# Optimization experiments

Hardware: AMD Instinct MI355X
Metric: run time of the kernel (lower is better)

Reference implementation:

```python
import jax, jax.numpy as jnp
import numpy as np

M = 2048      # mention groups (spans with antecedents)
K_MAX = 128   # max antecedents per mention
N = 4096      # candidate span pool
G = 1000      # span representation dim
D = 20        # distance/genre/speaker embed dim
H = 150       # Score MLP hidden
GIJ = 3 * G + 3 * D  # 3060


def setup_inputs() -> dict:
    key = jax.random.key(0)
    ks = jax.random.split(key, 12)
    # ragged group lengths (deterministic): cycle 1..K_MAX, sum = P = 132096
    lengths = np.tile(np.arange(1, K_MAX + 1), M // K_MAX).astype(np.int32)
    P = int(lengths.sum())
    seg_ids = np.repeat(np.arange(M), lengths).astype(np.int32)
    starts = np.cumsum(lengths) - lengths
    offsets = (np.arange(P) - starts[seg_ids]).astype(np.int32)

    genre_emb = jax.random.normal(ks[3], (8, D), jnp.float32) * 0.02
    genre_emb = genre_emb.at[0].set(0.0)   # padding_idx=0
    speaker_emb = jax.random.normal(ks[4], (3, D), jnp.float32) * 0.02
    speaker_emb = speaker_emb.at[0].set(0.0)  # padding_idx=0

    return {
        "g_i": jax.random.normal(ks[0], (N, G), jnp.float32),
        "mention_scores": jax.random.normal(ks[1], (N, 1), jnp.float32),
        "dist_emb": jax.random.normal(ks[2], (9, D), jnp.float32) * 0.02,
        "genre_emb": genre_emb,
        "speaker_emb": speaker_emb,
        "W1": jax.random.normal(ks[5], (GIJ, H), jnp.float32) / np.sqrt(GIJ),
        "b1": jnp.zeros((H,), jnp.float32),
        "W2": jax.random.normal(ks[6], (H, H), jnp.float32) / np.sqrt(H),
        "b2": jnp.zeros((H,), jnp.float32),
        "W3": jax.random.normal(ks[7], (H, 1), jnp.float32) / np.sqrt(H),
        "b3": jnp.zeros((1,), jnp.float32),
        "mention_ids": jax.random.randint(ks[8], (P,), 0, N, jnp.int32),
        "antecedent_ids": jax.random.randint(ks[9], (P,), 0, N, jnp.int32),
        "dist_ids": jax.random.randint(ks[10], (P,), 0, 9, jnp.int32),
        "genre_ids": jax.random.randint(ks[11], (P,), 0, 8, jnp.int32),
        "speaker_ids": jax.random.randint(jax.random.fold_in(key, 99), (P,), 0, 3, jnp.int32),
        "lengths": jnp.asarray(lengths),
        "seg_ids": jnp.asarray(seg_ids),
        "offsets": jnp.asarray(offsets),
    }


def reference(g_i, mention_scores, dist_emb, genre_emb, speaker_emb,
              W1, b1, W2, b2, W3, b3,
              mention_ids, antecedent_ids, dist_ids, genre_ids, speaker_ids,
              lengths, seg_ids, offsets):
    # feature gathers: phi = [distance, genre, speaker] embeddings, (P, 3D)
    phi = jnp.concatenate(
        [dist_emb[dist_ids], genre_emb[genre_ids], speaker_emb[speaker_ids]], axis=1)
    i_g = g_i[mention_ids]      # (P, G)
    j_g = g_i[antecedent_ids]   # (P, G)
    pairs = jnp.concatenate([i_g, j_g, i_g * j_g, phi], axis=1)  # (P, GIJ)

    # 3-layer scoring MLP (dropout inactive at eval)
    h = jax.nn.relu(pairs @ W1 + b1)
    h = jax.nn.relu(h @ W2 + b2)
    s_ij = (h @ W3 + b3)[:, 0]  # (P,)

    scores = mention_scores[mention_ids, 0] + mention_scores[antecedent_ids, 0] + s_ij

    # per-group softmax over [group scores, epsilon=0] via segment ops
    seg_max = jax.ops.segment_max(scores, seg_ids, num_segments=M)
    m = jnp.maximum(seg_max, 0.0)                      # include epsilon 0
    e = jnp.exp(scores - m[seg_ids])                   # (P,)
    eps_e = jnp.exp(-m)                                # (M,)
    denom = jax.ops.segment_sum(e, seg_ids, num_segments=M) + eps_e
    pair_probs = e / denom[seg_ids]                    # (P,)
    eps_probs = eps_e / denom                          # (M,)

    # pad_and_stack(value=1000): row 0 is the empty leading group -> [1, 1000...]
    grid = jnp.full((M + 1, K_MAX + 1), 1000.0, dtype=scores.dtype)
    grid = grid.at[seg_ids + 1, offsets].set(pair_probs)
    grid = grid.at[jnp.arange(M) + 1, lengths].set(eps_probs)
    grid = grid.at[0, 0].set(1.0)
    return grid
```

## Files before the change

### kernel.cpp

```cpp
#include <hip/hip_runtime.h>

#define P_TOTAL 132096
#define NPOOL   4096
#define GDIM    1000
#define HDIM    150
#define MGRP    2048
#define KMAX    128

typedef __attribute__((ext_vector_type(4))) float f32x4;
typedef __attribute__((ext_vector_type(2))) float f32x2;
typedef __attribute__((ext_vector_type(4))) unsigned int u32x4;

#define OFF_W1C8   0
#define OFF_W1AB8  163840
#define OFF_W2F8   491520
#define OFF_ABPRE  517120
#define OFF_TABS2  3138560
#define OFF_SGRID  3276800
#define OFF_GF8    4325376
#define OFF_ITAB   8519680

__device__ __forceinline__ short f2bf(float f) {
  union { float f; unsigned u; } v; v.f = f;
  unsigned r = v.u + 0x7FFFu + ((v.u >> 16) & 1u);
  return (short)(r >> 16);
}
__device__ __forceinline__ float bf2f(unsigned short s) {
  return __builtin_bit_cast(float, ((unsigned)s) << 16);
}
__device__ __forceinline__ unsigned char f2fp8(float f) {
  int d = __builtin_amdgcn_cvt_pk_fp8_f32(f, 0.f, 0, false);
  return (unsigned char)(d & 0xFF);
}
__device__ __forceinline__ long mk64(unsigned lo, unsigned hi) {
  return (long)(((unsigned long long)hi << 32) | lo);
}

__device__ __forceinline__ u32x4 fp8prod16(u32x4 m, u32x4 a) {
  u32x4 r;
  #pragma unroll
  for (int d = 0; d < 4; ++d) {
    f32x2 ml = __builtin_amdgcn_cvt_pk_f32_fp8(m[d], false);
    f32x2 mh = __builtin_amdgcn_cvt_pk_f32_fp8(m[d], true);
    f32x2 al = __builtin_amdgcn_cvt_pk_f32_fp8(a[d], false);
    f32x2 ah = __builtin_amdgcn_cvt_pk_f32_fp8(a[d], true);
    f32x2 pl = ml * al, ph = mh * ah;
    int o = __builtin_amdgcn_cvt_pk_fp8_f32(pl[0], pl[1], 0, false);
    o = __builtin_amdgcn_cvt_pk_fp8_f32(ph[0], ph[1], o, true);
    r[d] = (unsigned)o;
  }
  return r;
}

#define S1 5120
#define S2 10240
#define S3 800
#define S4 (NPOOL*256)
#define S5 (216*160)
#define S6 P_TOTAL
__global__ __launch_bounds__(256) void prep_kernel(
    const float* __restrict__ W1, const float* __restrict__ W2,
    const float* __restrict__ g_i,
    const float* __restrict__ dist_emb, const float* __restrict__ genre_emb,
    const float* __restrict__ spk_emb, const float* __restrict__ b1,
    const int* __restrict__ did, const int* __restrict__ gid,
    const int* __restrict__ sid,
    unsigned char* __restrict__ w1c8, unsigned char* __restrict__ w1ab8,
    unsigned char* __restrict__ w2f8, unsigned* __restrict__ gf8,
    float* __restrict__ tabs2, unsigned char* __restrict__ itab8) {
  int idx = blockIdx.x * 256 + threadIdx.x;
  if (idx < S1) {
    int c = idx / 160, n = idx % 160;
    int s = c >> 1, j = c & 1;
    unsigned dw[8];
    #pragma unroll
    for (int d = 0; d < 8; ++d) {
      unsigned acc = 0;
      #pragma unroll
      for (int b = 0; b < 4; ++b) {
        int kk = d*4 + b;
        int g = kk >> 3, i = kk & 7;
        int q = g ^ ((n >> 2) & 3);
        int k = s*64 + q*16 + j*8 + i;
        float v = (k < GDIM && n < HDIM) ? W1[(2000 + k)*HDIM + n] : 0.f;
        acc |= ((unsigned)f2fp8(v)) << (8*b);
      }
      dw[d] = acc;
    }
    u32x4 lo = {dw[0], dw[1], dw[2], dw[3]};
    u32x4 hi = {dw[4], dw[5], dw[6], dw[7]};
    *(u32x4*)(w1c8 + c*5120 + n*32)      = lo;
    *(u32x4*)(w1c8 + c*5120 + n*32 + 16) = hi;
  } else if (idx < S1 + S2) {
    int i2 = idx - S1;
    int c = i2 / 320, n = i2 % 320;
    int s = c >> 2, j = c & 3;
    unsigned dw[8];
    #pragma unroll
    for (int d = 0; d < 8; ++d) {
      unsigned acc = 0;
      #pragma unroll
      for (int b = 0; b < 4; ++b) {
        int kk = d*4 + b;
        int g = kk >> 3, i = kk & 7;
        int k = s*128 + g*32 + j*8 + i;
        float v = 0.f;
        if (k < GDIM) {
          if (n < HDIM)                 v = W1[k*HDIM + n];
          else if (n >= 160 && n < 310) v = W1[(1000 + k)*HDIM + (n - 160)];
        }
        acc |= ((unsigned)f2fp8(v)) << (8*b);
      }
      dw[d] = acc;
    }
    u32x4 lo = {dw[0], dw[1], dw[2], dw[3]};
    u32x4 hi = {dw[4], dw[5], dw[6], dw[7]};
    *(u32x4*)(w1ab8 + c*10240 + n*32)      = lo;
    *(u32x4*)(w1ab8 + c*10240 + n*32 + 16) = hi;
  } else if (idx < S1 + S2 + S3) {
    int i2 = idx - S1 - S2;
    int c = i2 / 160, n = i2 % 160;
    unsigned dw[8];
    #pragma unroll
    for (int d = 0; d < 8; ++d) {
      unsigned acc = 0;
      #pragma unroll
      for (int b = 0; b < 4; ++b) {
        int kk = d*4 + b;
        int g = kk >> 3, ii = kk & 7;
        int q = g ^ ((n >> 2) & 3);
        int k = c*32 + q*8 + ii;
        float v = (k < HDIM && n < HDIM) ? W2[k*HDIM + n] : 0.f;
        acc |= ((unsigned)f2fp8(v)) << (8*b);
      }
      dw[d] = acc;
    }
    u32x4 lo = {dw[0], dw[1], dw[2], dw[3]};
    u32x4 hi = {dw[4], dw[5], dw[6], dw[7]};
    *(u32x4*)(w2f8 + c*5120 + n*32)      = lo;
    *(u32x4*)(w2f8 + c*5120 + n*32 + 16) = hi;
  } else if (idx < S1 + S2 + S3 + S4) {
    int i = idx - S1 - S2 - S3;
    int row = i >> 8, jd = i & 255;
    int c0 = jd * 4;
    float f0 = (c0     < GDIM) ? g_i[row*GDIM + c0]     : 0.f;
    float f1 = (c0 + 1 < GDIM) ? g_i[row*GDIM + c0 + 1] : 0.f;
    float f2 = (c0 + 2 < GDIM) ? g_i[row*GDIM + c0 + 2] : 0.f;
    float f3 = (c0 + 3 < GDIM) ? g_i[row*GDIM + c0 + 3] : 0.f;
    int d = 0;
    d = __builtin_amdgcn_cvt_pk_fp8_f32(f0, f1, d, false);
    d = __builtin_amdgcn_cvt_pk_fp8_f32(f2, f3, d, true);
    gf8[i] = (unsigned)d;
  } else if (idx < S1 + S2 + S3 + S4 + S5) {
    int i = idx - S1 - S2 - S3 - S4;
    int row = i / 160, n = i % 160;
    float acc = 0.f;
    if (n < HDIM) {
      int d = row / 24, g = (row / 3) % 8, sp = row % 3;
      acc = b1[n];
      #pragma unroll
      for (int kk = 0; kk < 20; ++kk) {
        acc += dist_emb [d*20 + kk]  * W1[(3000 + kk)*HDIM + n];
        acc += genre_emb[g*20 + kk]  * W1[(3020 + kk)*HDIM + n];
        acc += spk_emb  [sp*20 + kk] * W1[(3040 + kk)*HDIM + n];
      }
    }
    tabs2[i] = acc;
  } else if (idx < S1 + S2 + S3 + S4 + S5 + S6) {
    int p = idx - (S1 + S2 + S3 + S4 + S5);
    itab8[p] = (unsigned char)(did[p]*24 + gid[p]*3 + sid[p]);
  }
}

__global__ __launch_bounds__(128) void pre_gemm_kernel(
    const unsigned char* __restrict__ gf8, const unsigned char* __restrict__ w1ab8,
    unsigned short* __restrict__ abpre) {
  int wave = threadIdx.x >> 6, lane = threadIdx.x & 63;
  int quad = lane >> 4, n16 = lane & 15;
  int rowbase = blockIdx.x * 32 + wave * 16;
  int colbase = blockIdx.y * 80;

  f32x4 acc[5];
  #pragma unroll
  for (int t = 0; t < 5; ++t) acc[t] = (f32x4){0.f, 0.f, 0.f, 0.f};

  const unsigned char* arow = gf8 + (long)(rowbase + n16) * 1024 + quad*32;

  for (int s = 0; s < 8; ++s) {
    u32x4 Aa = *(const u32x4*)(arow + s*128);
    u32x4 Ab = *(const u32x4*)(arow + s*128 + 16);
    #pragma unroll
    for (int j = 0; j < 4; ++j) {
      long a = (j == 0) ? mk64(Aa[0], Aa[1]) : (j == 1) ? mk64(Aa[2], Aa[3])
             : (j == 2) ? mk64(Ab[0], Ab[1]) : mk64(Ab[2], Ab[3]);
      const unsigned char* bp = w1ab8 + (((s*4 + j)*320 + colbase + n16) * 32 + quad*8);
      #pragma unroll
      for (int t = 0; t < 5; ++t) {
        long b = *(const long*)(bp + t*16*32);
        acc[t] = __builtin_amdgcn_mfma_f32_16x16x32_fp8_fp8(a, b, acc[t], 0, 0, 0);
      }
    }
  }
  #pragma unroll
  for (int t = 0; t < 5; ++t) {
    #pragma unroll
    for (int r = 0; r < 4; ++r) {
      int row = rowbase + quad*4 + r;
      abpre[(long)row * 320 + colbase + t*16 + n16] = (unsigned short)f2bf(acc[t][r]);
    }
  }
}

__global__ __launch_bounds__(256) void mlp_kernel(
    const unsigned char* __restrict__ gf8,
    const unsigned short* __restrict__ abpre,
    const float* __restrict__ tabs2,
    const unsigned char* __restrict__ itab8,
    const unsigned char* __restrict__ w1c8,
    const unsigned char* __restrict__ w2f8,
    const float* __restrict__ ms,
    const float* __restrict__ W3, const float* __restrict__ b2,
    const float* __restrict__ b3,
    const int* __restrict__ mention_ids, const int* __restrict__ antecedent_ids,
    const int* __restrict__ seg_ids, const int* __restrict__ offs,
    float* __restrict__ sgrid) {

  __shared__ __align__(16) unsigned char lds[53248];

  int tid = threadIdx.x;
  int wave = tid >> 6, lane = tid & 63;
  int quad = lane >> 4, n16 = lane & 15;
  int lp0 = blockIdx.x * 128;
  int gp0 = lp0;
  int wrow = wave * 32;

  int jj = (lane & 3) ^ ((lane >> 2) & 3) ^ ((lane >> 4) & 1);
  int srow = lane >> 2;
  int swA = quad ^ (n16 & 3) ^ ((n16 >> 2) & 1);
  int swB = quad ^ ((n16 >> 2) & 3);

  const unsigned char* pA0 =
      gf8 + (long)mention_ids[gp0 + wave*16 + srow] * 1024 + jj*16;
  const unsigned char* pA1 =
      gf8 + (long)mention_ids[gp0 + (wave + 4)*16 + srow] * 1024 + jj*16;
  const unsigned char* pA2 =
      gf8 + (long)antecedent_ids[gp0 + wave*16 + srow] * 1024 + jj*16;
  const unsigned char* pA3 =
      gf8 + (long)antecedent_ids[gp0 + (wave + 4)*16 + srow] * 1024 + jj*16;
  int dA0 = wave*1024,      dA1 = (wave + 4)*1024;
  int dA2 = 8192 + dA0,     dA3 = 8192 + dA1;

  f32x4 acc0[10], acc1[10];
  #pragma unroll
  for (int t = 0; t < 10; ++t) {
    acc0[t] = (f32x4){0.f, 0.f, 0.f, 0.f};
    acc1[t] = (f32x4){0.f, 0.f, 0.f, 0.f};
  }

  auto issue = [&](int s, int buf) {
    unsigned char* base = lds + buf*26624;
    long so = (long)s * 64;
    __builtin_amdgcn_global_load_lds((const unsigned int*)(pA0 + so),
        (unsigned int*)(base + dA0 + lane*16), 16, 0, 0);
    __builtin_amdgcn_global_load_lds((const unsigned int*)(pA1 + so),
        (unsigned int*)(base + dA1 + lane*16), 16, 0, 0);
    __builtin_amdgcn_global_load_lds((const unsigned int*)(pA2 + so),
        (unsigned int*)(base + dA2 + lane*16), 16, 0, 0);
    __builtin_amdgcn_global_load_lds((const unsigned int*)(pA3 + so),
        (unsigned int*)(base + dA3 + lane*16), 16, 0, 0);
    const unsigned char* wsrc = w1c8 + (long)s*10240;
    __builtin_amdgcn_global_load_lds((const unsigned int*)(wsrc + wave*1024 + (long)lane*16),
        (unsigned int*)(base + 16384 + wave*1024 + lane*16), 16, 0, 0);
    __builtin_amdgcn_global_load_lds((const unsigned int*)(wsrc + (wave+4)*1024 + (long)lane*16),
        (unsigned int*)(base + 16384 + (wave+4)*1024 + lane*16), 16, 0, 0);
    if (wave < 2)
      __builtin_amdgcn_global_load_lds((const unsigned int*)(wsrc + (wave+8)*1024 + (long)lane*16),
          (unsigned int*)(base + 16384 + (wave+8)*1024 + lane*16), 16, 0, 0);
  };

  issue(0, 0);
  for (int s = 0; s < 16; ++s) {
    __syncthreads();
    if (s < 15) issue(s + 1, (s + 1) & 1);
    const unsigned char* cb = lds + (s & 1)*26624;

    u32x4 M0 = *(const u32x4*)(cb + (wrow + n16)*64 + swA*16);
    u32x4 C0 = *(const u32x4*)(cb + 8192 + (wrow + n16)*64 + swA*16);
    u32x4 M1 = *(const u32x4*)(cb + (wrow + 16 + n16)*64 + swA*16);
    u32x4 C1 = *(const u32x4*)(cb + 8192 + (wrow + 16 + n16)*64 + swA*16);
    u32x4 P0 = fp8prod16(M0, C0);
    u32x4 P1 = fp8prod16(M1, C1);

    #pragma unroll
    for (int j = 0; j < 2; ++j) {
      long a0 = (j == 0) ? mk64(P0[0], P0[1]) : mk64(P0[2], P0[3]);
      long a1 = (j == 0) ? mk64(P1[0], P1[1]) : mk64(P1[2], P1[3]);
      const unsigned char* bp = cb + 16384 + j*5120 + n16*32 + swB*8;
      #pragma unroll
      for (int t = 0; t < 10; ++t) {
        long b = *(const long*)(bp + t*512);
        acc0[t] = __builtin_amdgcn_mfma_f32_16x16x32_fp8_fp8(a0, b, acc0[t], 0, 0, 0);
        acc1[t] = __builtin_amdgcn_mfma_f32_16x16x32_fp8_fp8(a1, b, acc1[t], 0, 0, 0);
      }
    }
  }
  __syncthreads();

  for (int r = wave; r < 25; r += 4) {
    __builtin_amdgcn_global_load_lds(
        (const unsigned int*)(w2f8 + r*1024 + (long)lane*16),
        (unsigned int*)(lds + 26624 + r*1024), 16, 0, 0);
  }

  unsigned char* h1w = lds + wave * 5888;
  #pragma unroll
  for (int r = 0; r < 4; ++r) {
    int row0 = quad*4 + r;
    int gpA = gp0 + wrow + row0;
    int gpB = gpA + 16;
    const unsigned short* pmA = abpre + (long)mention_ids[gpA]*320;
    const unsigned short* paA = abpre + (long)antecedent_ids[gpA]*320 + 160;
    const float*          tbA = tabs2 + (long)itab8[gpA]*160;
    const unsigned short* pmB = abpre + (long)mention_ids[gpB]*320;
    const unsigned short* paB = abpre + (long)antecedent_ids[gpB]*320 + 160;
    const float*          tbB = tabs2 + (long)itab8[gpB]*160;
    #pragma unroll
    for (int t = 0; t < 10; ++t) {
      int n = t*16 + n16;
      float v0 = acc0[t][r] + bf2f(pmA[n]) + bf2f(paA[n]) + tbA[n];
      float v1 = acc1[t][r] + bf2f(pmB[n]) + bf2f(paB[n]) + tbB[n];
      h1w[row0*184 + n]        = f2fp8(fmaxf(v0, 0.f));
      h1w[(16 + row0)*184 + n] = f2fp8(fmaxf(v1, 0.f));
    }
  }
  __syncthreads();

  float bias3 = b3[0];
  float w3v[10], b2v[10];
  #pragma unroll
  for (int t = 0; t < 10; ++t) {
    int n = t*16 + n16;
    w3v[t] = (n < HDIM) ? W3[n] : 0.f;
    b2v[t] = (n < HDIM) ? b2[n] : 0.f;
  }

  #pragma unroll
  for (int tile = 0; tile < 2; ++tile) {
    f32x4 acc2[10];
    #pragma unroll
    for (int t = 0; t < 10; ++t) acc2[t] = (f32x4){0.f, 0.f, 0.f, 0.f};

    #pragma unroll
    for (int c = 0; c < 5; ++c) {
      long a = *(const long*)(h1w + (tile*16 + n16)*184 + c*32 + quad*8);
      const unsigned char* bp = lds + 26624 + (c*160 + n16)*32 + swB*8;
      #pragma unroll
      for (int t = 0; t < 10; ++t) {
        long b = *(const long*)(bp + t*512);
        acc2[t] = __builtin_amdgcn_mfma_f32_16x16x32_fp8_fp8(a, b, acc2[t], 0, 0, 0);
      }
    }

    float part[4] = {0.f, 0.f, 0.f, 0.f};
    #pragma unroll
    for (int t = 0; t < 10; ++t) {
      #pragma unroll
      for (int r = 0; r < 4; ++r) {
        float h2 = fmaxf(acc2[t][r] + b2v[t], 0.f);
        part[r] += h2 * w3v[t];
      }
    }
    for (int msk = 1; msk < 16; msk <<= 1) {
      #pragma unroll
      for (int r = 0; r < 4; ++r) part[r] += __shfl_xor(part[r], msk);
    }

    if (n16 == 0) {
      #pragma unroll
      for (int r = 0; r < 4; ++r) {
        int gp = gp0 + wrow + tile*16 + quad*4 + r;
        float sc = part[r] + bias3 + ms[mention_ids[gp]] + ms[antecedent_ids[gp]];
        sgrid[seg_ids[gp] * KMAX + offs[gp]] = sc;
      }
    }
  }
}

__global__ __launch_bounds__(128) void softmax_kernel(const float* __restrict__ sgrid,
                                                      const int* __restrict__ lengths,
                                                      float* __restrict__ out) {
  int b = blockIdx.x, t = threadIdx.x;
  if (b == 0) {
    out[t] = (t == 0) ? 1.0f : 1000.0f;
    if (t == 0) out[128] = 1000.0f;
    return;
  }
  int m = b - 1;
  int len = lengths[m];
  float s = (t < len) ? sgrid[m * KMAX + t] : -1e30f;

  __shared__ float redA[2];
  __shared__ float redB[2];

  float v = s;
  #pragma unroll
  for (int o = 32; o >= 1; o >>= 1) v = fmaxf(v, __shfl_xor(v, o));
  if ((t & 63) == 0) redA[t >> 6] = v;
  __syncthreads();
  float mx = fmaxf(fmaxf(redA[0], redA[1]), 0.0f);

  float e = (t < len) ? expf(s - mx) : 0.f;
  float sum = e;
  #pragma unroll
  for (int o = 32; o >= 1; o >>= 1) sum += __shfl_xor(sum, o);
  if ((t & 63) == 0) redB[t >> 6] = sum;
  __syncthreads();

  float eps_e = expf(-mx);
  float denom = redB[0] + redB[1] + eps_e;

  float* row = out + (long)(m + 1) * 129;
  float val;
  if (t < len)       val = e / denom;
  else if (t == len) val = eps_e / denom;
  else               val = 1000.0f;
  row[t] = val;
  if (t == 0) row[128] = (len == KMAX) ? (eps_e / denom) : 1000.0f;
}

extern "C" void kernel_launch(void* const* d_in, const int* in_sizes, int n_in,
                              void* d_out, int out_size, void* d_ws, size_t ws_size,
                              hipStream_t stream) {
  const float* g_i        = (const float*)d_in[0];
  const float* ms         = (const float*)d_in[1];
  const float* dist_emb   = (const float*)d_in[2];
  const float* genre_emb  = (const float*)d_in[3];
  const float* spk_emb    = (const float*)d_in[4];
  const float* W1         = (const float*)d_in[5];
  const float* b1         = (const float*)d_in[6];
  const float* W2         = (const float*)d_in[7];
  const float* b2         = (const float*)d_in[8];
  const float* W3         = (const float*)d_in[9];
  const float* b3         = (const float*)d_in[10];
  const int* mention_ids    = (const int*)d_in[11];
  const int* antecedent_ids = (const int*)d_in[12];
  const int* dist_ids       = (const int*)d_in[13];
  const int* genre_ids      = (const int*)d_in[14];
  const int* spk_ids        = (const int*)d_in[15];
  const int* lengths        = (const int*)d_in[16];
  const int* seg_ids        = (const int*)d_in[17];
  const int* offsets        = (const int*)d_in[18];

  char* ws = (char*)d_ws;
  unsigned char* w1c8  = (unsigned char*)(ws + OFF_W1C8);
  unsigned char* w1ab8 = (unsigned char*)(ws + OFF_W1AB8);
  unsigned char* w2f8  = (unsigned char*)(ws + OFF_W2F8);
  unsigned short* abpre = (unsigned short*)(ws + OFF_ABPRE);
  float* tabs2  = (float*)(ws + OFF_TABS2);
  float* sgrid  = (float*)(ws + OFF_SGRID);
  unsigned char* gf8  = (unsigned char*)(ws + OFF_GF8);
  unsigned char* itab8 = (unsigned char*)(ws + OFF_ITAB);

  const int prepN = S1 + S2 + S3 + S4 + S5 + S6;
  prep_kernel<<<(prepN + 255)/256, 256, 0, stream>>>(W1, W2, g_i,
                                                     dist_emb, genre_emb, spk_emb, b1,
                                                     dist_ids, genre_ids, spk_ids,
                                                     w1c8, w1ab8, w2f8,
                                                     (unsigned*)gf8, tabs2, itab8);
  dim3 gpre(NPOOL/32, 4);
  pre_gemm_kernel<<<gpre, 128, 0, stream>>>(gf8, w1ab8, abpre);
  mlp_kernel<<<P_TOTAL/128, 256, 0, stream>>>(gf8, abpre, tabs2, itab8,
                                              w1c8, w2f8, ms,
                                              W3, b2, b3,
                                              mention_ids, antecedent_ids,
                                              seg_ids, offsets, sgrid);
  softmax_kernel<<<MGRP + 1, 128, 0, stream>>>(sgrid, lengths, (float*)d_out);
}
```

Measured before the change: 199.7 us.

## Vectorize gathered layer-1 partial sums via LDS staging and retile pre-GEMM

The mlp kernel now gathers the per-pair mention/antecedent precomputed rows and the categorical table with 16-byte vector loads, four lanes per row. It sums them in fp32, packs the result to bf16, and stages it in LDS before adding it to the MFMA accumulators. This replaces scattered 2-byte per-lane gathers. The W2 tile moves to a lower LDS offset so it shares space with the staging buffer, which adds extra barriers. The pre-GEMM kernel is retiled to one 16x16 output tile per wave on a larger grid, which exposes more parallelism but gives less B-operand reuse per wave.

```diff
diff --git a/kernel.cpp b/kernel.cpp
--- a/kernel.cpp
+++ b/kernel.cpp
@@ -50,6 +50,12 @@
     r[d] = (unsigned)o;
   }
   return r;
+}
+
+__device__ __forceinline__ unsigned pk_bf16(float lo, float hi) {
+  unsigned o;
+  asm("v_cvt_pk_bf16_f32 %0, %1, %2" : "=v"(o) : "v"(lo), "v"(hi));
+  return o;
 }
 
 #define S1 5120
@@ -172,48 +178,32 @@
   }
 }
 
-__global__ __launch_bounds__(128) void pre_gemm_kernel(
+__global__ __launch_bounds__(256) void pre_gemm_kernel(
     const unsigned char* __restrict__ gf8, const unsigned char* __restrict__ w1ab8,
     unsigned short* __restrict__ abpre) {
   int wave = threadIdx.x >> 6, lane = threadIdx.x & 63;
   int quad = lane >> 4, n16 = lane & 15;
-  int rowbase = blockIdx.x * 32 + wave * 16;
-  int colbase = blockIdx.y * 80;
-
-  f32x4 acc[5];
-  #pragma unroll
-  for (int t = 0; t < 5; ++t) acc[t] = (f32x4){0.f, 0.f, 0.f, 0.f};
-
-  const unsigned char* arow = gf8 + (long)(rowbase + n16) * 1024 + quad*32;
-
-  for (int s = 0; s < 8; ++s) {
-    u32x4 Aa = *(const u32x4*)(arow + s*128);
-    u32x4 Ab = *(const u32x4*)(arow + s*128 + 16);
-    #pragma unroll
-    for (int j = 0; j < 4; ++j) {
-      long a = (j == 0) ? mk64(Aa[0], Aa[1]) : (j == 1) ? mk64(Aa[2], Aa[3])
-             : (j == 2) ? mk64(Ab[0], Ab[1]) : mk64(Ab[2], Ab[3]);
-      const unsigned char* bp = w1ab8 + (((s*4 + j)*320 + colbase + n16) * 32 + quad*8);
-      #pragma unroll
-      for (int t = 0; t < 5; ++t) {
-        long b = *(const long*)(bp + t*16*32);
-        acc[t] = __builtin_amdgcn_mfma_f32_16x16x32_fp8_fp8(a, b, acc[t], 0, 0, 0);
-      }
-    }
-  }
-  #pragma unroll
-  for (int t = 0; t < 5; ++t) {
-    #pragma unroll
-    for (int r = 0; r < 4; ++r) {
-      int row = rowbase + quad*4 + r;
-      abpre[(long)row * 320 + colbase + t*16 + n16] = (unsigned short)f2bf(acc[t][r]);
-    }
-  }
+  int row0 = blockIdx.x * 64 + wave * 16;
+  int col0 = blockIdx.y * 16;
+
+  f32x4 acc = (f32x4){0.f, 0.f, 0.f, 0.f};
+  const unsigned char* arow  = gf8 + (long)(row0 + n16) * 1024 + quad*32;
+  const unsigned char* bbase = w1ab8 + ((long)col0 + n16) * 32 + quad*8;
+
+  #pragma unroll 4
+  for (int c = 0; c < 32; ++c) {
+    long a = *(const long*)(arow + (c >> 2)*128 + (c & 3)*8);
+    long b = *(const long*)(bbase + (long)c * 10240);
+    acc = __builtin_amdgcn_mfma_f32_16x16x32_fp8_fp8(a, b, acc, 0, 0, 0);
+  }
+  #pragma unroll
+  for (int r = 0; r < 4; ++r)
+    abpre[(long)(row0 + quad*4 + r) * 320 + col0 + n16] = (unsigned short)f2bf(acc[r]);
 }
 
 __global__ __launch_bounds__(256) void mlp_kernel(
     const unsigned char* __restrict__ gf8,
-    const unsigned short* __restrict__ abpre,
+    const unsigned* __restrict__ abpre32,
     const float* __restrict__ tabs2,
     const unsigned char* __restrict__ itab8,
     const unsigned char* __restrict__ w1c8,
@@ -306,34 +296,56 @@
   }
   __syncthreads();
 
+  unsigned* extw = (unsigned*)(lds + 23552 + wave*5376);
+  const unsigned short* ext16 = (const unsigned short*)extw;
+  unsigned char* h1w = lds + wave * 5888;
+  int rowi = lane >> 2, q4 = lane & 3;
+
+  #pragma unroll
+  for (int p = 0; p < 2; ++p) {
+    int gpe = gp0 + wrow + p*16 + rowi;
+    int m  = mention_ids[gpe];
+    int a  = antecedent_ids[gpe];
+    int it = itab8[gpe];
+    const u32x4* pm = (const u32x4*)(abpre32 + (long)m*160 + q4*20);
+    const u32x4* pa = (const u32x4*)(abpre32 + (long)a*160 + 80 + q4*20);
+    const f32x4* tb = (const f32x4*)(tabs2 + (long)it*160 + q4*40);
+    #pragma unroll
+    for (int k = 0; k < 5; ++k) {
+      u32x4 um = pm[k], ua = pa[k];
+      f32x4 ta = tb[2*k], tc = tb[2*k + 1];
+      u32x4 ov;
+      #pragma unroll
+      for (int d = 0; d < 4; ++d) {
+        float f0 = (d == 0) ? ta[0] : (d == 1) ? ta[2] : (d == 2) ? tc[0] : tc[2];
+        float f1 = (d == 0) ? ta[1] : (d == 1) ? ta[3] : (d == 2) ? tc[1] : tc[3];
+        float v0 = bf2f((unsigned short)(um[d] & 0xffff))
+                 + bf2f((unsigned short)(ua[d] & 0xffff)) + f0;
+        float v1 = bf2f((unsigned short)(um[d] >> 16))
+                 + bf2f((unsigned short)(ua[d] >> 16)) + f1;
+        ov[d] = pk_bf16(v0, v1);
+      }
+      *(u32x4*)(extw + rowi*84 + q4*20 + 4*k) = ov;
+    }
+    #pragma unroll
+    for (int r = 0; r < 4; ++r) {
+      int lr = quad*4 + r;
+      #pragma unroll
+      for (int t = 0; t < 10; ++t) {
+        int n = t*16 + n16;
+        float e = bf2f(ext16[lr*168 + n]);
+        float v = ((p == 0) ? acc0[t][r] : acc1[t][r]) + e;
+        h1w[(p*16 + lr)*184 + n] = f2fp8(fmaxf(v, 0.f));
+      }
+    }
+    __syncthreads();
+  }
+
   for (int r = wave; r < 25; r += 4) {
     __builtin_amdgcn_global_load_lds(
         (const unsigned int*)(w2f8 + r*1024 + (long)lane*16),
-        (unsigned int*)(lds + 26624 + r*1024), 16, 0, 0);
-  }
-
-  unsigned char* h1w = lds + wave * 5888;
-  #pragma unroll
-  for (int r = 0; r < 4; ++r) {
-    int row0 = quad*4 + r;
-    int gpA = gp0 + wrow + row0;
-    int gpB = gpA + 16;
-    const unsigned short* pmA = abpre + (long)mention_ids[gpA]*320;
-    const unsigned short* paA = abpre + (long)antecedent_ids[gpA]*320 + 160;
-    const float*          tbA = tabs2 + (long)itab8[gpA]*160;
-    const unsigned short* pmB = abpre + (long)mention_ids[gpB]*320;
-    const unsigned short* paB = abpre + (long)antecedent_ids[gpB]*320 + 160;
-    const float*          tbB = tabs2 + (long)itab8[gpB]*160;
-    #pragma unroll
-    for (int t = 0; t < 10; ++t) {
-      int n = t*16 + n16;
-      float v0 = acc0[t][r] + bf2f(pmA[n]) + bf2f(paA[n]) + tbA[n];
-      float v1 = acc1[t][r] + bf2f(pmB[n]) + bf2f(paB[n]) + tbB[n];
-      h1w[row0*184 + n]        = f2fp8(fmaxf(v0, 0.f));
-      h1w[(16 + row0)*184 + n] = f2fp8(fmaxf(v1, 0.f));
-    }
-  }
-  __syncthreads();
+        (unsigned int*)(lds + 23552 + r*1024), 16, 0, 0);
+  }
 
   float bias3 = b3[0];
   float w3v[10], b2v[10];
@@ -343,6 +355,7 @@
     w3v[t] = (n < HDIM) ? W3[n] : 0.f;
     b2v[t] = (n < HDIM) ? b2[n] : 0.f;
   }
+  __syncthreads();
 
   #pragma unroll
   for (int tile = 0; tile < 2; ++tile) {
@@ -353,7 +366,7 @@
     #pragma unroll
     for (int c = 0; c < 5; ++c) {
       long a = *(const long*)(h1w + (tile*16 + n16)*184 + c*32 + quad*8);
-      const unsigned char* bp = lds + 26624 + (c*160 + n16)*32 + swB*8;
+      const unsigned char* bp = lds + 23552 + (c*160 + n16)*32 + swB*8;
       #pragma unroll
       for (int t = 0; t < 10; ++t) {
         long b = *(const long*)(bp + t*512);
@@ -467,9 +480,9 @@
                                                      dist_ids, genre_ids, spk_ids,
                                                      w1c8, w1ab8, w2f8,
                                                      (unsigned*)gf8, tabs2, itab8);
-  dim3 gpre(NPOOL/32, 4);
-  pre_gemm_kernel<<<gpre, 128, 0, stream>>>(gf8, w1ab8, abpre);
-  mlp_kernel<<<P_TOTAL/128, 256, 0, stream>>>(gf8, abpre, tabs2, itab8,
+  dim3 gpre(NPOOL/64, 20);
+  pre_gemm_kernel<<<gpre, 256, 0, stream>>>(gf8, w1ab8, abpre);
+  mlp_kernel<<<P_TOTAL/128, 256, 0, stream>>>(gf8, (const unsigned*)abpre, tabs2, itab8,
                                               w1c8, w2f8, ms,
                                               W3, b2, b3,
                                               mention_ids, antecedent_ids,
```

Result: slower. 214.2 us (+7.3%).
